# Kernel optimization log

Hardware: AMD Instinct MI355X
Metric: run time of the kernel (lower is better)

The kernel has to match this reference:

```python
import jax, jax.numpy as jnp
import numpy as np

H_FWD, H_REV, M = 25, 25, 3        # n=3, m=3 hardcoded in module
IN_SIZE = 4 * H_REV + 1            # 101 = H_rev + (n-2) + H_rev*m
UNITS = 512
BATCH = 8192
INPUT_SIZE = H_REV + (3 - 2) + (H_FWD + H_REV) * M  # 176


def setup_inputs() -> dict:
    key = jax.random.key(0)
    ks = jax.random.split(key, 6)
    x = jax.random.normal(ks[0], (BATCH, INPUT_SIZE), jnp.float32)

    def lin(k, fi, fo):
        kw, kb = jax.random.split(k)
        W = jax.random.normal(kw, (fi, fo), jnp.float32) / np.float32(np.sqrt(fi))
        b = jax.random.normal(kb, (fo,), jnp.float32) * 0.01
        return W, b

    W0, b0 = lin(ks[1], IN_SIZE, UNITS)
    W1, b1 = lin(ks[2], UNITS, UNITS)
    W2, b2 = lin(ks[3], UNITS, UNITS)
    W3, b3 = lin(ks[4], UNITS, UNITS)
    W4, b4 = lin(ks[5], UNITS, 1)
    return dict(x=x, W0=W0, b0=b0, W1=W1, b1=b1, W2=W2, b2=b2,
                W3=W3, b3=b3, W4=W4, b4=b4)


def _mlp(params, d):
    # Tanh MLP, final Linear to scalar; returns (B,)
    h = d
    for W, b in params[:-1]:
        h = jnp.tanh(h @ W + b)
    W, b = params[-1]
    return (h @ W + b)[:, 0]


def reference(x, W0, b0, W1, b1, W2, b2, W3, b3, W4, b4):
    params = [(W0, b0), (W1, b1), (W2, b2), (W3, b3), (W4, b4)]
    B = x.shape[0]
    e = x[:, :H_REV]                                   # (B, H_rev)
    v = x[:, -(H_FWD + H_REV) * M:].reshape(B, H_FWD + H_REV, M)
    f = lambda d: _mlp(params, d)

    w_cols, grads = [], []
    for i in range(H_FWD):  # strictly sequential recursion over horizon
        if i < H_REV:
            if i > 0:
                w_seg = jax.lax.stop_gradient(jnp.stack(w_cols, axis=1))
            else:
                w_seg = jnp.zeros((B, 0), x.dtype)
            data = jnp.concatenate(
                [e[:, i:], w_seg,
                 v[:, i:i + H_REV].reshape(B, -1),
                 jnp.full((B, 1), float(i), x.dtype)], axis=1)
        else:
            w_seg = jax.lax.stop_gradient(jnp.stack(w_cols[i - H_REV:i], axis=1))
            data = jnp.concatenate(
                [w_seg, v[:, i:i + H_REV].reshape(B, -1),
                 jnp.full((B, 1), float(i), x.dtype)], axis=1)
        out, vjp_fn = jax.vjp(f, data)      # out: (B,), scalar output per sample
        g, = vjp_fn(jnp.ones_like(out))     # (B, IN_SIZE): per-step Jacobian row
        w_cols.append(out)
        grads.append(g)

    w = jnp.stack(w_cols, axis=1)           # (B, H_fwd)
    grad = jnp.stack(grads, axis=1)         # (B, H_fwd, IN_SIZE)
    return w, grad
```

## Files before the change

kernel.cpp:

```cpp
#include <hip/hip_runtime.h>

#define B_ROWS 8192
#define UNITS 512
#define NITER 25
#define INSZ 176
#define KPAD 128
#define GRAD_COLS 101

typedef __attribute__((ext_vector_type(8))) short short8;
typedef __attribute__((ext_vector_type(4))) float f32x4;
typedef __attribute__((ext_vector_type(8))) _Float16 half8;

__device__ __forceinline__ unsigned short f2h_bits(float f) {
  _Float16 h = (_Float16)f;
  return __builtin_bit_cast(unsigned short, h);
}
__device__ __forceinline__ float h2f_bits(unsigned short b) {
  return (float)__builtin_bit_cast(_Float16, b);
}
__device__ __forceinline__ float fast_tanh(float x) {
  float e = __expf(2.0f * x);
  return 1.0f - 2.0f / (e + 1.0f);
}

typedef __attribute__((address_space(3))) unsigned int lds_u32;
typedef __attribute__((address_space(1))) const unsigned int glb_u32;
__device__ __forceinline__ void gload16(const void* g, void* l) {
  __builtin_amdgcn_global_load_lds((glb_u32*)g, (lds_u32*)l, 16, 0, 0);
}

struct GArgs {
  const unsigned short *A;
  const unsigned short *B;
  int K;
  const float* bias;
  const unsigned short *Hh;
  unsigned short *Oh;
  float* Og;
  int iter;
};

__global__ __launch_bounds__(256)
void prep_kernel(const float* __restrict__ W0, const float* __restrict__ W1,
                 const float* __restrict__ W2, const float* __restrict__ W3,
                 unsigned short* TW0, unsigned short* TW1,
                 unsigned short* TW2, unsigned short* TW3,
                 unsigned short* CW0, unsigned short* CW1,
                 unsigned short* CW2, unsigned short* CW3)
{
  int id = blockIdx.x * 256 + threadIdx.x;
  if (id < 512 * KPAD) {
    int n = id >> 7, k = id & (KPAD - 1);
    TW0[id] = f2h_bits((k < 101) ? W0[(size_t)k * 512 + n] : 0.0f);
    int n2 = id >> 9, k2 = id & 511;
    CW0[id] = f2h_bits((n2 < 101) ? W0[(size_t)n2 * 512 + k2] : 0.0f);
  }
  {
    int n = id >> 9, k = id & 511;
    TW1[id] = f2h_bits(W1[(size_t)k * 512 + n]);
    TW2[id] = f2h_bits(W2[(size_t)k * 512 + n]);
    TW3[id] = f2h_bits(W3[(size_t)k * 512 + n]);
    CW1[id] = f2h_bits(W1[id]);
    CW2[id] = f2h_bits(W2[id]);
    CW3[id] = f2h_bits(W3[id]);
  }
}

__global__ __launch_bounds__(256)
void build_d_kernel(const float* __restrict__ x, unsigned short* __restrict__ D)
{
  int id = blockIdx.x * 256 + threadIdx.x;
  int b = id >> 7, c = id & 127;
  float val;
  if (c < 25)             val = x[(size_t)b * INSZ + c];
  else if (c < 100)       val = x[(size_t)b * INSZ + 26 + (c - 25)];
  else                    val = 0.0f;
  D[id] = f2h_bits(val);
}

template<int EPI>
__device__ __forceinline__ void gemm_body(const GArgs g, short* smem, int id)
{
  const int t = threadIdx.x;
  const int w = t >> 6;
  const int lane = t & 63;
  const int l15 = lane & 15, l4 = lane >> 4;
  const int bm = (EPI == 2) ? id : ((id & 7) | ((id >> 5) << 3));
  const int bn = (EPI == 2) ? 0  : ((id >> 3) & 3);
  const int wm = (w >> 1) * 64, wn = (w & 1) * 64;
  const int K = g.K;
  const int NK = K >> 6;
  f32x4 acc[4][4] = {};

  const int sr = t >> 3;
  const int ss = t & 7;

  auto stage = [&](int ks, int buf) {
    short* As = smem + buf * 16384;
    short* Bs = As + 8192;
    int kc = ks << 6;
#pragma unroll
    for (int q = 0; q < 4; ++q) {
      int r = q * 32 + sr;
      int c = ss ^ (r & 7);
      size_t ga = (size_t)(bm * 128 + r) * K + kc + c * 8;
      size_t gb = (size_t)(bn * 128 + r) * K + kc + c * 8;
      int ldst = q * 2048 + w * 512;
      gload16(g.A + ga, &As[ldst]);
      gload16(g.B + gb, &Bs[ldst]);
    }
  };

  stage(0, 0);

  for (int ks = 0; ks < NK; ++ks) {
    if (ks + 1 < NK) {
      stage(ks + 1, (ks + 1) & 1);
      asm volatile("s_waitcnt vmcnt(8)" ::: "memory");
    } else {
      asm volatile("s_waitcnt vmcnt(0)" ::: "memory");
    }
    __builtin_amdgcn_sched_barrier(0);
    __builtin_amdgcn_s_barrier();

    const short* As = smem + (ks & 1) * 16384;
    const short* Bs = As + 8192;
#pragma unroll
    for (int kk = 0; kk < 2; ++kk) {
      short8 av[4], bh[4];
#pragma unroll
      for (int mi = 0; mi < 4; ++mi) {
        int row = wm + mi * 16 + l15;
        int eoff = row * 64 + (((kk * 4 + l4) ^ (row & 7)) << 3);
        av[mi] = *(const short8*)&As[eoff];
      }
#pragma unroll
      for (int ni = 0; ni < 4; ++ni) {
        int row = wn + ni * 16 + l15;
        int eoff = row * 64 + (((kk * 4 + l4) ^ (row & 7)) << 3);
        bh[ni] = *(const short8*)&Bs[eoff];
      }
#pragma unroll
      for (int mi = 0; mi < 4; ++mi)
#pragma unroll
        for (int ni = 0; ni < 4; ++ni)
          acc[mi][ni] = __builtin_amdgcn_mfma_f32_16x16x32_f16(
              __builtin_bit_cast(half8, av[mi]), __builtin_bit_cast(half8, bh[ni]),
              acc[mi][ni], 0, 0, 0);
    }
    asm volatile("s_waitcnt lgkmcnt(0)" ::: "memory");
    __builtin_amdgcn_sched_barrier(0);
    __builtin_amdgcn_s_barrier();
  }

  const int gm0 = bm * 128 + wm;
  const int gn0 = bn * 128 + wn;
#pragma unroll
  for (int mi = 0; mi < 4; ++mi) {
#pragma unroll
    for (int ni = 0; ni < 4; ++ni) {
      int n = gn0 + ni * 16 + l15;
#pragma unroll
      for (int r = 0; r < 4; ++r) {
        int m = gm0 + mi * 16 + l4 * 4 + r;
        float v = acc[mi][ni][r];
        if constexpr (EPI == 0) {
          float h = fast_tanh(v + g.bias[n]);
          g.Oh[(size_t)m * UNITS + n] = f2h_bits(h);
        } else if constexpr (EPI == 1) {
          size_t idx = (size_t)m * UNITS + n;
          float h = h2f_bits(g.Hh[idx]);
          g.Oh[idx] = f2h_bits(v * (1.0f - h * h));
        } else {
          if (n < GRAD_COLS)
            g.Og[((size_t)m * NITER + g.iter) * GRAD_COLS + n] = v;
        }
      }
    }
  }
}

template<int EA, int EB>
__global__ __launch_bounds__(256, 2)
void paired_kernel(GArgs A, GArgs B, int nA) {
  __shared__ short smem[32768];
  int id = blockIdx.x;
  if (id < nA) gemm_body<EA>(A, smem, id);
  else         gemm_body<EB>(B, smem, id - nA);
}

template<int E>
__global__ __launch_bounds__(256, 2)
void solo_kernel(GArgs A) {
  __shared__ short smem[32768];
  gemm_body<E>(A, smem, blockIdx.x);
}

__global__ __launch_bounds__(256)
void dot_bd_kernel(const unsigned short* __restrict__ H3,
                   const float* __restrict__ W4, const float* __restrict__ b4,
                   const float* __restrict__ x, float* __restrict__ w_out,
                   unsigned short* __restrict__ U,
                   unsigned short* __restrict__ D,
                   int iter, int buildD)
{
  int w = threadIdx.x >> 6, lane = threadIdx.x & 63;
  int b = blockIdx.x * 4 + w;
  size_t base = (size_t)b * UNITS + lane * 8;
  short8 vh = *(const short8*)&H3[base];
  float dot = 0.0f;
  short8 ou;
#pragma unroll
  for (int j = 0; j < 8; ++j) {
    float h = h2f_bits((unsigned short)vh[j]);
    float g = W4[lane * 8 + j];
    dot += h * g;
    ou[j] = (short)f2h_bits((1.0f - h * h) * g);
  }
  *(short8*)&U[base] = ou;
#pragma unroll
  for (int off = 1; off < 64; off <<= 1) dot += __shfl_xor(dot, off);
  float wv = dot + b4[0];
  if (lane == 0) w_out[(size_t)b * NITER + iter] = wv;

  if (buildD) {
    int jn = iter + 1;
#pragma unroll
    for (int cc = 0; cc < 2; ++cc) {
      int c = lane + cc * 64;
      float val;
      if (c < 25 - jn)        val = x[(size_t)b * INSZ + jn + c];
      else if (c < 24)        val = w_out[(size_t)b * NITER + (c - (25 - jn))];
      else if (c == 24)       val = wv;
      else if (c < 100)       val = x[(size_t)b * INSZ + 26 + 3 * jn + (c - 25)];
      else if (c == 100)      val = (float)jn;
      else                    val = 0.0f;
      D[(size_t)b * KPAD + c] = f2h_bits(val);
    }
  }
}

extern "C" void kernel_launch(void* const* d_in, const int* in_sizes, int n_in,
                              void* d_out, int out_size, void* d_ws, size_t ws_size,
                              hipStream_t stream) {
  const float* x  = (const float*)d_in[0];
  const float* W0 = (const float*)d_in[1];
  const float* b0 = (const float*)d_in[2];
  const float* W1 = (const float*)d_in[3];
  const float* b1 = (const float*)d_in[4];
  const float* W2 = (const float*)d_in[5];
  const float* b2 = (const float*)d_in[6];
  const float* W3 = (const float*)d_in[7];
  const float* b3 = (const float*)d_in[8];
  const float* W4 = (const float*)d_in[9];
  const float* b4 = (const float*)d_in[10];

  float* w_out    = (float*)d_out;
  float* grad_out = (float*)d_out + (size_t)B_ROWS * NITER;

  char* p = (char*)d_ws;
  auto alloc = [&](size_t elems) { unsigned short* r = (unsigned short*)p; p += elems * 2; return r; };

  unsigned short* TW0 = alloc(512 * KPAD);
  unsigned short* TW1 = alloc(512 * 512);
  unsigned short* TW2 = alloc(512 * 512);
  unsigned short* TW3 = alloc(512 * 512);
  unsigned short* CW0 = alloc(KPAD * 512);
  unsigned short* CW1 = alloc(512 * 512);
  unsigned short* CW2 = alloc(512 * 512);
  unsigned short* CW3 = alloc(512 * 512);

  unsigned short* D = alloc((size_t)B_ROWS * KPAD);

  unsigned short *H[2][4];
  for (int par = 0; par < 2; ++par)
    for (int l = 0; l < 4; ++l)
      H[par][l] = alloc((size_t)B_ROWS * UNITS);
  unsigned short* Ua = alloc((size_t)B_ROWS * UNITS);
  unsigned short* Ub = alloc((size_t)B_ROWS * UNITS);

  prep_kernel<<<1024, 256, 0, stream>>>(W0, W1, W2, W3,
      TW0, TW1, TW2, TW3, CW0, CW1, CW2, CW3);

  build_d_kernel<<<4096, 256, 0, stream>>>(x, D);

  {
    GArgs f0 = {D, TW0, KPAD, b0, nullptr, H[0][0], nullptr, 0};
    GArgs f1 = {H[0][0], TW1, 512, b1, nullptr, H[0][1], nullptr, 0};
    GArgs f2 = {H[0][1], TW2, 512, b2, nullptr, H[0][2], nullptr, 0};
    GArgs f3 = {H[0][2], TW3, 512, b3, nullptr, H[0][3], nullptr, 0};
    solo_kernel<0><<<256, 256, 0, stream>>>(f0);
    solo_kernel<0><<<256, 256, 0, stream>>>(f1);
    solo_kernel<0><<<256, 256, 0, stream>>>(f2);
    solo_kernel<0><<<256, 256, 0, stream>>>(f3);
  }

  for (int i = 0; i < NITER; ++i) {
    int pp = i & 1, q = pp ^ 1;
    bool more = (i < NITER - 1);

    dot_bd_kernel<<<2048, 256, 0, stream>>>(H[pp][3], W4, b4, x, w_out,
                                            Ua, D, i, more ? 1 : 0);

    GArgs bw3 = {Ua, CW3, 512, nullptr, H[pp][2], Ub, nullptr, 0};
    GArgs bw2 = {Ub, CW2, 512, nullptr, H[pp][1], Ua, nullptr, 0};
    GArgs bw1 = {Ua, CW1, 512, nullptr, H[pp][0], Ub, nullptr, 0};
    GArgs gr0 = {Ub, CW0, 512, nullptr, nullptr, nullptr, grad_out, i};

    if (more) {
      GArgs f0 = {D, TW0, KPAD, b0, nullptr, H[q][0], nullptr, 0};
      GArgs f1 = {H[q][0], TW1, 512, b1, nullptr, H[q][1], nullptr, 0};
      GArgs f2 = {H[q][1], TW2, 512, b2, nullptr, H[q][2], nullptr, 0};
      GArgs f3 = {H[q][2], TW3, 512, b3, nullptr, H[q][3], nullptr, 0};
      paired_kernel<1, 0><<<512, 256, 0, stream>>>(bw3, f0, 256);
      paired_kernel<1, 0><<<512, 256, 0, stream>>>(bw2, f1, 256);
      paired_kernel<1, 0><<<512, 256, 0, stream>>>(bw1, f2, 256);
      paired_kernel<2, 0><<<320, 256, 0, stream>>>(gr0, f3, 64);
    } else {
      solo_kernel<1><<<256, 256, 0, stream>>>(bw3);
      solo_kernel<1><<<256, 256, 0, stream>>>(bw2);
      solo_kernel<1><<<256, 256, 0, stream>>>(bw1);
      solo_kernel<2><<<64, 256, 0, stream>>>(gr0);
    }
  }

  (void)in_sizes; (void)n_in; (void)out_size; (void)ws_size;
}
```

Baseline: 1.961 ms.

## Batch backward passes across forward iterations into large chunked GEMMs

The sequential forward recursion now runs alone, with the final W4 dot product and the dtanh*W4 seed fused into the last forward GEMM epilogue through atomics into a zeroed accumulator. The backward chain for several iterations (up to all 25 if workspace allows) is then run as one large GEMM per layer over stacked activations, replacing the per-iteration paired forward/backward launches. Forward GEMMs use 64-row tiles to keep more blocks in flight. This needs much more workspace and adds atomic float sums, which can change rounding order.

Result: slower. 2.001 ms (+2.0%).

```diff
diff --git a/kernel.cpp b/kernel.cpp
--- a/kernel.cpp
+++ b/kernel.cpp
@@ -27,6 +27,11 @@
 typedef __attribute__((address_space(1))) const unsigned int glb_u32;
 __device__ __forceinline__ void gload16(const void* g, void* l) {
   __builtin_amdgcn_global_load_lds((glb_u32*)g, (lds_u32*)l, 16, 0, 0);
+}
+
+__device__ __forceinline__ f32x4 mf(short8 a, short8 b, f32x4 c) {
+  return __builtin_amdgcn_mfma_f32_16x16x32_f16(
+      __builtin_bit_cast(half8, a), __builtin_bit_cast(half8, b), c, 0, 0, 0);
 }
 
 struct GArgs {
@@ -38,6 +43,7 @@
   unsigned short *Oh;
   float* Og;
   int iter;
+  const float* W4p;
 };
 
 __global__ __launch_bounds__(256)
@@ -46,9 +52,11 @@
                  unsigned short* TW0, unsigned short* TW1,
                  unsigned short* TW2, unsigned short* TW3,
                  unsigned short* CW0, unsigned short* CW1,
-                 unsigned short* CW2, unsigned short* CW3)
+                 unsigned short* CW2, unsigned short* CW3,
+                 float* w_acc)
 {
   int id = blockIdx.x * 256 + threadIdx.x;
+  if (id < NITER * B_ROWS) w_acc[id] = 0.0f;
   if (id < 512 * KPAD) {
     int n = id >> 7, k = id & (KPAD - 1);
     TW0[id] = f2h_bits((k < 101) ? W0[(size_t)k * 512 + n] : 0.0f);
@@ -67,7 +75,7 @@
 }
 
 __global__ __launch_bounds__(256)
-void build_d_kernel(const float* __restrict__ x, unsigned short* __restrict__ D)
+void build_d0_kernel(const float* __restrict__ x, unsigned short* __restrict__ D)
 {
   int id = blockIdx.x * 256 + threadIdx.x;
   int b = id >> 7, c = id & 127;
@@ -79,12 +87,131 @@
 }
 
 template<int EPI>
-__device__ __forceinline__ void gemm_body(const GArgs g, short* smem, int id)
+__global__ __launch_bounds__(256, 2)
+void fwd_kernel(GArgs g)
 {
+  __shared__ short smem[24576];
   const int t = threadIdx.x;
   const int w = t >> 6;
   const int lane = t & 63;
   const int l15 = lane & 15, l4 = lane >> 4;
+  const int id = blockIdx.x;
+  const int bm = (id & 7) | ((id >> 5) << 3);
+  const int bn = (id >> 3) & 3;
+  const int wm = (w >> 1) * 32, wn = (w & 1) * 64;
+  const int K = g.K;
+  const int NK = K >> 6;
+  f32x4 acc[2][4] = {};
+
+  const int sr = t >> 3;
+  const int ss = t & 7;
+
+  auto stage = [&](int ks, int buf) {
+    short* As = smem + buf * 12288;
+    short* Bs = As + 4096;
+    int kc = ks << 6;
+#pragma unroll
+    for (int q = 0; q < 2; ++q) {
+      int r = q * 32 + sr;
+      int c = ss ^ (r & 7);
+      size_t ga = (size_t)(bm * 64 + r) * K + kc + c * 8;
+      gload16(g.A + ga, &As[q * 2048 + w * 512]);
+    }
+#pragma unroll
+    for (int q = 0; q < 4; ++q) {
+      int r = q * 32 + sr;
+      int c = ss ^ (r & 7);
+      size_t gb = (size_t)(bn * 128 + r) * K + kc + c * 8;
+      gload16(g.B + gb, &Bs[q * 2048 + w * 512]);
+    }
+  };
+
+  stage(0, 0);
+  for (int ks = 0; ks < NK; ++ks) {
+    if (ks + 1 < NK) {
+      stage(ks + 1, (ks + 1) & 1);
+      asm volatile("s_waitcnt vmcnt(6)" ::: "memory");
+    } else {
+      asm volatile("s_waitcnt vmcnt(0)" ::: "memory");
+    }
+    __builtin_amdgcn_sched_barrier(0);
+    __builtin_amdgcn_s_barrier();
+
+    const short* As = smem + (ks & 1) * 12288;
+    const short* Bs = As + 4096;
+#pragma unroll
+    for (int kk = 0; kk < 2; ++kk) {
+      short8 av[2], bh[4];
+#pragma unroll
+      for (int mi = 0; mi < 2; ++mi) {
+        int row = wm + mi * 16 + l15;
+        av[mi] = *(const short8*)&As[row * 64 + (((kk * 4 + l4) ^ (row & 7)) << 3)];
+      }
+#pragma unroll
+      for (int ni = 0; ni < 4; ++ni) {
+        int row = wn + ni * 16 + l15;
+        bh[ni] = *(const short8*)&Bs[row * 64 + (((kk * 4 + l4) ^ (row & 7)) << 3)];
+      }
+#pragma unroll
+      for (int mi = 0; mi < 2; ++mi)
+#pragma unroll
+        for (int ni = 0; ni < 4; ++ni)
+          acc[mi][ni] = mf(av[mi], bh[ni], acc[mi][ni]);
+    }
+    asm volatile("s_waitcnt lgkmcnt(0)" ::: "memory");
+    __builtin_amdgcn_sched_barrier(0);
+    __builtin_amdgcn_s_barrier();
+  }
+
+  const int gm0 = bm * 64 + wm;
+  const int gn0 = bn * 128 + wn;
+  float wp[2][4] = {};
+#pragma unroll
+  for (int mi = 0; mi < 2; ++mi) {
+#pragma unroll
+    for (int ni = 0; ni < 4; ++ni) {
+      int n = gn0 + ni * 16 + l15;
+#pragma unroll
+      for (int r = 0; r < 4; ++r) {
+        int m = gm0 + mi * 16 + l4 * 4 + r;
+        float v = acc[mi][ni][r];
+        float h = fast_tanh(v + g.bias[n]);
+        if constexpr (EPI == 0) {
+          g.Oh[(size_t)m * UNITS + n] = f2h_bits(h);
+        } else {
+          float w4 = g.W4p[n];
+          g.Oh[(size_t)m * UNITS + n] = f2h_bits((1.0f - h * h) * w4);
+          wp[mi][r] += h * w4;
+        }
+      }
+    }
+  }
+  if constexpr (EPI == 3) {
+#pragma unroll
+    for (int mi = 0; mi < 2; ++mi)
+#pragma unroll
+      for (int r = 0; r < 4; ++r) {
+        float v = wp[mi][r];
+        v += __shfl_xor(v, 1); v += __shfl_xor(v, 2);
+        v += __shfl_xor(v, 4); v += __shfl_xor(v, 8);
+        if (l15 == 0) {
+          int m = gm0 + mi * 16 + l4 * 4 + r;
+          atomicAdd(&g.Og[m], v);
+        }
+      }
+  }
+}
+
+template<int EPI>
+__global__ __launch_bounds__(256, 2)
+void bwd_kernel(GArgs g)
+{
+  __shared__ short smem[32768];
+  const int t = threadIdx.x;
+  const int w = t >> 6;
+  const int lane = t & 63;
+  const int l15 = lane & 15, l4 = lane >> 4;
+  const int id = blockIdx.x;
   const int bm = (EPI == 2) ? id : ((id & 7) | ((id >> 5) << 3));
   const int bn = (EPI == 2) ? 0  : ((id >> 3) & 3);
   const int wm = (w >> 1) * 64, wn = (w & 1) * 64;
@@ -112,7 +239,6 @@
   };
 
   stage(0, 0);
-
   for (int ks = 0; ks < NK; ++ks) {
     if (ks + 1 < NK) {
       stage(ks + 1, (ks + 1) & 1);
@@ -131,22 +257,18 @@
 #pragma unroll
       for (int mi = 0; mi < 4; ++mi) {
         int row = wm + mi * 16 + l15;
-        int eoff = row * 64 + (((kk * 4 + l4) ^ (row & 7)) << 3);
-        av[mi] = *(const short8*)&As[eoff];
+        av[mi] = *(const short8*)&As[row * 64 + (((kk * 4 + l4) ^ (row & 7)) << 3)];
       }
 #pragma unroll
       for (int ni = 0; ni < 4; ++ni) {
         int row = wn + ni * 16 + l15;
-        int eoff = row * 64 + (((kk * 4 + l4) ^ (row & 7)) << 3);
-        bh[ni] = *(const short8*)&Bs[eoff];
+        bh[ni] = *(const short8*)&Bs[row * 64 + (((kk * 4 + l4) ^ (row & 7)) << 3)];
       }
 #pragma unroll
       for (int mi = 0; mi < 4; ++mi)
 #pragma unroll
         for (int ni = 0; ni < 4; ++ni)
-          acc[mi][ni] = __builtin_amdgcn_mfma_f32_16x16x32_f16(
-              __builtin_bit_cast(half8, av[mi]), __builtin_bit_cast(half8, bh[ni]),
-              acc[mi][ni], 0, 0, 0);
+          acc[mi][ni] = mf(av[mi], bh[ni], acc[mi][ni]);
     }
     asm volatile("s_waitcnt lgkmcnt(0)" ::: "memory");
     __builtin_amdgcn_sched_barrier(0);
@@ -164,79 +286,40 @@
       for (int r = 0; r < 4; ++r) {
         int m = gm0 + mi * 16 + l4 * 4 + r;
         float v = acc[mi][ni][r];
-        if constexpr (EPI == 0) {
-          float h = fast_tanh(v + g.bias[n]);
-          g.Oh[(size_t)m * UNITS + n] = f2h_bits(h);
-        } else if constexpr (EPI == 1) {
+        if constexpr (EPI == 1) {
           size_t idx = (size_t)m * UNITS + n;
           float h = h2f_bits(g.Hh[idx]);
           g.Oh[idx] = f2h_bits(v * (1.0f - h * h));
         } else {
-          if (n < GRAD_COLS)
-            g.Og[((size_t)m * NITER + g.iter) * GRAD_COLS + n] = v;
+          if (n < GRAD_COLS) {
+            int it = m >> 13, b = m & 8191;
+            g.Og[((size_t)b * NITER + (g.iter + it)) * GRAD_COLS + n] = v;
+          }
         }
       }
     }
   }
 }
 
-template<int EA, int EB>
-__global__ __launch_bounds__(256, 2)
-void paired_kernel(GArgs A, GArgs B, int nA) {
-  __shared__ short smem[32768];
-  int id = blockIdx.x;
-  if (id < nA) gemm_body<EA>(A, smem, id);
-  else         gemm_body<EB>(B, smem, id - nA);
-}
-
-template<int E>
-__global__ __launch_bounds__(256, 2)
-void solo_kernel(GArgs A) {
-  __shared__ short smem[32768];
-  gemm_body<E>(A, smem, blockIdx.x);
-}
-
 __global__ __launch_bounds__(256)
-void dot_bd_kernel(const unsigned short* __restrict__ H3,
-                   const float* __restrict__ W4, const float* __restrict__ b4,
-                   const float* __restrict__ x, float* __restrict__ w_out,
-                   unsigned short* __restrict__ U,
-                   unsigned short* __restrict__ D,
-                   int iter, int buildD)
+void build_dw_kernel(const float* __restrict__ x, const float* __restrict__ w_acc,
+                     const float* __restrict__ b4, float* __restrict__ w_out,
+                     unsigned short* __restrict__ D, int iter)
 {
-  int w = threadIdx.x >> 6, lane = threadIdx.x & 63;
-  int b = blockIdx.x * 4 + w;
-  size_t base = (size_t)b * UNITS + lane * 8;
-  short8 vh = *(const short8*)&H3[base];
-  float dot = 0.0f;
-  short8 ou;
-#pragma unroll
-  for (int j = 0; j < 8; ++j) {
-    float h = h2f_bits((unsigned short)vh[j]);
-    float g = W4[lane * 8 + j];
-    dot += h * g;
-    ou[j] = (short)f2h_bits((1.0f - h * h) * g);
-  }
-  *(short8*)&U[base] = ou;
-#pragma unroll
-  for (int off = 1; off < 64; off <<= 1) dot += __shfl_xor(dot, off);
-  float wv = dot + b4[0];
-  if (lane == 0) w_out[(size_t)b * NITER + iter] = wv;
-
-  if (buildD) {
+  int id = blockIdx.x * 256 + threadIdx.x;
+  int b = id >> 7, c = id & 127;
+  float wv = w_acc[(size_t)iter * B_ROWS + b] + b4[0];
+  if (c == 0) w_out[(size_t)b * NITER + iter] = wv;
+  if (iter < NITER - 1) {
     int jn = iter + 1;
-#pragma unroll
-    for (int cc = 0; cc < 2; ++cc) {
-      int c = lane + cc * 64;
-      float val;
-      if (c < 25 - jn)        val = x[(size_t)b * INSZ + jn + c];
-      else if (c < 24)        val = w_out[(size_t)b * NITER + (c - (25 - jn))];
-      else if (c == 24)       val = wv;
-      else if (c < 100)       val = x[(size_t)b * INSZ + 26 + 3 * jn + (c - 25)];
-      else if (c == 100)      val = (float)jn;
-      else                    val = 0.0f;
-      D[(size_t)b * KPAD + c] = f2h_bits(val);
-    }
+    float val;
+    if (c < 25 - jn)        val = x[(size_t)b * INSZ + jn + c];
+    else if (c < 24)        val = w_out[(size_t)b * NITER + (c - (25 - jn))];
+    else if (c == 24)       val = wv;
+    else if (c < 100)       val = x[(size_t)b * INSZ + 26 + 3 * jn + (c - 25)];
+    else if (c == 100)      val = (float)jn;
+    else                    val = 0.0f;
+    D[(size_t)b * KPAD + c] = f2h_bits(val);
   }
 }
 
@@ -258,6 +341,17 @@
   float* w_out    = (float*)d_out;
   float* grad_out = (float*)d_out + (size_t)B_ROWS * NITER;
 
+  const size_t SL    = (size_t)B_ROWS * UNITS;
+  const size_t FIXED = 3407872 + 2097152 + 819200 + 4096;
+  int CH = 1;
+  {
+    const int lad[4] = {25, 5, 3, 2};
+    for (int k = 0; k < 4; ++k) {
+      size_t need = FIXED + (size_t)lad[k] * 5 * SL * 2;
+      if (ws_size >= need) { CH = lad[k]; break; }
+    }
+  }
+
   char* p = (char*)d_ws;
   auto alloc = [&](size_t elems) { unsigned short* r = (unsigned short*)p; p += elems * 2; return r; };
 
@@ -269,60 +363,46 @@
   unsigned short* CW1 = alloc(512 * 512);
   unsigned short* CW2 = alloc(512 * 512);
   unsigned short* CW3 = alloc(512 * 512);
-
-  unsigned short* D = alloc((size_t)B_ROWS * KPAD);
-
-  unsigned short *H[2][4];
-  for (int par = 0; par < 2; ++par)
-    for (int l = 0; l < 4; ++l)
-      H[par][l] = alloc((size_t)B_ROWS * UNITS);
-  unsigned short* Ua = alloc((size_t)B_ROWS * UNITS);
-  unsigned short* Ub = alloc((size_t)B_ROWS * UNITS);
+  unsigned short* D   = alloc((size_t)B_ROWS * KPAD);
+  float* w_acc = (float*)p; p += (size_t)NITER * B_ROWS * 4;
+
+  unsigned short* H0w = alloc((size_t)CH * SL);
+  unsigned short* H1w = alloc((size_t)CH * SL);
+  unsigned short* H2w = alloc((size_t)CH * SL);
+  unsigned short* U3w = alloc((size_t)CH * SL);
+  unsigned short* Ubw = alloc((size_t)CH * SL);
 
   prep_kernel<<<1024, 256, 0, stream>>>(W0, W1, W2, W3,
-      TW0, TW1, TW2, TW3, CW0, CW1, CW2, CW3);
-
-  build_d_kernel<<<4096, 256, 0, stream>>>(x, D);
-
-  {
-    GArgs f0 = {D, TW0, KPAD, b0, nullptr, H[0][0], nullptr, 0};
-    GArgs f1 = {H[0][0], TW1, 512, b1, nullptr, H[0][1], nullptr, 0};
-    GArgs f2 = {H[0][1], TW2, 512, b2, nullptr, H[0][2], nullptr, 0};
-    GArgs f3 = {H[0][2], TW3, 512, b3, nullptr, H[0][3], nullptr, 0};
-    solo_kernel<0><<<256, 256, 0, stream>>>(f0);
-    solo_kernel<0><<<256, 256, 0, stream>>>(f1);
-    solo_kernel<0><<<256, 256, 0, stream>>>(f2);
-    solo_kernel<0><<<256, 256, 0, stream>>>(f3);
-  }
-
-  for (int i = 0; i < NITER; ++i) {
-    int pp = i & 1, q = pp ^ 1;
-    bool more = (i < NITER - 1);
-
-    dot_bd_kernel<<<2048, 256, 0, stream>>>(H[pp][3], W4, b4, x, w_out,
-                                            Ua, D, i, more ? 1 : 0);
-
-    GArgs bw3 = {Ua, CW3, 512, nullptr, H[pp][2], Ub, nullptr, 0};
-    GArgs bw2 = {Ub, CW2, 512, nullptr, H[pp][1], Ua, nullptr, 0};
-    GArgs bw1 = {Ua, CW1, 512, nullptr, H[pp][0], Ub, nullptr, 0};
-    GArgs gr0 = {Ub, CW0, 512, nullptr, nullptr, nullptr, grad_out, i};
-
-    if (more) {
-      GArgs f0 = {D, TW0, KPAD, b0, nullptr, H[q][0], nullptr, 0};
-      GArgs f1 = {H[q][0], TW1, 512, b1, nullptr, H[q][1], nullptr, 0};
-      GArgs f2 = {H[q][1], TW2, 512, b2, nullptr, H[q][2], nullptr, 0};
-      GArgs f3 = {H[q][2], TW3, 512, b3, nullptr, H[q][3], nullptr, 0};
-      paired_kernel<1, 0><<<512, 256, 0, stream>>>(bw3, f0, 256);
-      paired_kernel<1, 0><<<512, 256, 0, stream>>>(bw2, f1, 256);
-      paired_kernel<1, 0><<<512, 256, 0, stream>>>(bw1, f2, 256);
-      paired_kernel<2, 0><<<320, 256, 0, stream>>>(gr0, f3, 64);
-    } else {
-      solo_kernel<1><<<256, 256, 0, stream>>>(bw3);
-      solo_kernel<1><<<256, 256, 0, stream>>>(bw2);
-      solo_kernel<1><<<256, 256, 0, stream>>>(bw1);
-      solo_kernel<2><<<64, 256, 0, stream>>>(gr0);
-    }
-  }
-
-  (void)in_sizes; (void)n_in; (void)out_size; (void)ws_size;
-}
+      TW0, TW1, TW2, TW3, CW0, CW1, CW2, CW3, w_acc);
+  build_d0_kernel<<<4096, 256, 0, stream>>>(x, D);
+
+  for (int j0 = 0; j0 < NITER; j0 += CH) {
+    int wlen = (NITER - j0 < CH) ? (NITER - j0) : CH;
+    for (int it = 0; it < wlen; ++it) {
+      int i = j0 + it;
+      unsigned short* H0s = H0w + (size_t)it * SL;
+      unsigned short* H1s = H1w + (size_t)it * SL;
+      unsigned short* H2s = H2w + (size_t)it * SL;
+      unsigned short* U3s = U3w + (size_t)it * SL;
+      GArgs f0 = {D,   TW0, KPAD, b0, nullptr, H0s, nullptr, 0, nullptr};
+      GArgs f1 = {H0s, TW1, 512,  b1, nullptr, H1s, nullptr, 0, nullptr};
+      GArgs f2 = {H1s, TW2, 512,  b2, nullptr, H2s, nullptr, 0, nullptr};
+      GArgs f3 = {H2s, TW3, 512,  b3, nullptr, U3s, w_acc + (size_t)i * B_ROWS, 0, W4};
+      fwd_kernel<0><<<512, 256, 0, stream>>>(f0);
+      fwd_kernel<0><<<512, 256, 0, stream>>>(f1);
+      fwd_kernel<0><<<512, 256, 0, stream>>>(f2);
+      fwd_kernel<3><<<512, 256, 0, stream>>>(f3);
+      build_dw_kernel<<<4096, 256, 0, stream>>>(x, w_acc, b4, w_out, D, i);
+    }
+    GArgs bw3 = {U3w, CW3, 512, nullptr, H2w, Ubw, nullptr, 0, nullptr};
+    GArgs bw2 = {Ubw, CW2, 512, nullptr, H1w, U3w, nullptr, 0, nullptr};
+    GArgs bw1 = {U3w, CW1, 512, nullptr, H0w, Ubw, nullptr, 0, nullptr};
+    GArgs gr0 = {Ubw, CW0, 512, nullptr, nullptr, nullptr, grad_out, j0, nullptr};
+    bwd_kernel<1><<<wlen * 256, 256, 0, stream>>>(bw3);
+    bwd_kernel<1><<<wlen * 256, 256, 0, stream>>>(bw2);
+    bwd_kernel<1><<<wlen * 256, 256, 0, stream>>>(bw1);
+    bwd_kernel<2><<<wlen * 64,  256, 0, stream>>>(gr0);
+  }
+
+  (void)in_sizes; (void)n_in; (void)out_size;
+}
```
